# Kernel tuning notes

Hardware: AMD Instinct MI355X
Metric: run time of the kernel (lower is better)

## Reference

```python
import jax, jax.numpy as jnp
import numpy as np

N_CANONICAL = 16
D_IN, D_HID, D_OUT = 784, 128, 10
BATCH = 65536


def setup_inputs() -> dict:
    key = jax.random.key(0)
    ks = jax.random.split(key, 6)
    x = jax.random.normal(ks[0], (BATCH, D_IN), dtype=jnp.float32)
    # per-canonical Linear params (PyTorch Linear: y = x @ W.T + b)
    s1 = 1.0 / np.sqrt(D_IN)
    s2 = 1.0 / np.sqrt(D_HID)
    fc_w = jax.random.uniform(ks[1], (N_CANONICAL, D_HID, D_IN), jnp.float32, -s1, s1)
    fc_b = jax.random.uniform(ks[2], (N_CANONICAL, D_HID), jnp.float32, -s1, s1)
    cls_w = jax.random.uniform(ks[3], (N_CANONICAL, D_OUT, D_HID), jnp.float32, -s2, s2)
    cls_b = jax.random.uniform(ks[4], (N_CANONICAL, D_OUT), jnp.float32, -s2, s2)
    factor = jnp.full((N_CANONICAL,), 1.0 / N_CANONICAL, dtype=jnp.float32)
    return {"x": x, "fc_w": fc_w, "fc_b": fc_b, "cls_w": cls_w, "cls_b": cls_b, "factor": factor}


def reference(x, fc_w, fc_b, cls_w, cls_b, factor):
    # x: [B, 784] (already flattened view of 28x28)
    # Ensemble of Linears combined by learned scalar factor. Since the combination
    # is linear, pre-combine weights: sum_k factor[k] * W_k (same math, fused GEMM).
    w1 = jnp.einsum('k,kod->od', factor, fc_w)   # [128, 784]
    b1 = factor @ fc_b                           # [128]
    h = jax.nn.relu(x @ w1.T + b1)               # [B, 128]
    w2 = jnp.einsum('k,kod->od', factor, cls_w)  # [10, 128]
    b2 = factor @ cls_b                          # [10]
    out = h @ w2.T + b2                          # [B, 10]
    return out
```

## Files before the change

### kernel.cpp

```cpp
#include <hip/hip_runtime.h>
#include <hip/hip_bf16.h>

typedef __attribute__((ext_vector_type(8))) short short8;
typedef __attribute__((ext_vector_type(4))) float f32x4;

#define N_ENS 16
#define D_IN 784
#define D_HID 128
#define D_OUT 10
#define KPAD 800
#define NKT 25
#define BM 64
#define TILE_B_BYTES 8192
#define WS_B1 204800
#define WS_W2 205312
#define WS_B2 210432

__device__ __forceinline__ unsigned short f2bf(float f) {
  unsigned int u = __float_as_uint(f);
  return (unsigned short)((u + 0x7FFFu + ((u >> 16) & 1u)) >> 16);
}

__device__ __forceinline__ void gload_lds16(const void* g, void* l) {
  __builtin_amdgcn_global_load_lds((const __attribute__((address_space(1))) void*)g,
                                   (__attribute__((address_space(3))) void*)l, 16, 0, 0);
}

__device__ __forceinline__ int swz(int row, int byte_in_row) {
  return ((row << 6) | byte_in_row) ^ ((row & 7) << 4);
}

__global__ void prep_kernel(const float* __restrict__ fc_w, const float* __restrict__ fc_b,
                            const float* __restrict__ cls_w, const float* __restrict__ cls_b,
                            const float* __restrict__ factor, char* __restrict__ ws) {
  int tid = blockIdx.x * 256 + threadIdx.x;
  float f[N_ENS];
#pragma unroll
  for (int e = 0; e < N_ENS; ++e) f[e] = factor[e];

  if (tid < D_HID * KPAD) {
    int col = tid / KPAD;
    int k   = tid - col * KPAD;
    float v = 0.f;
    if (k < D_IN) {
#pragma unroll
      for (int e = 0; e < N_ENS; ++e) v += f[e] * fc_w[(size_t)(e * D_HID + col) * D_IN + k];
    }
    int kt = k >> 5, kk = k & 31;
    *(unsigned short*)(ws + kt * TILE_B_BYTES + swz(col, kk * 2)) = f2bf(v);
  } else if (tid < D_HID * KPAD + D_HID) {
    int col = tid - D_HID * KPAD;
    float v = 0.f;
#pragma unroll
    for (int e = 0; e < N_ENS; ++e) v += f[e] * fc_b[e * D_HID + col];
    *(float*)(ws + WS_B1 + col * 4) = v;
  } else if (tid < D_HID * KPAD + D_HID + D_HID * D_OUT) {
    int i = tid - (D_HID * KPAD + D_HID);
    int n = i / D_OUT, o = i - n * D_OUT;
    float v = 0.f;
#pragma unroll
    for (int e = 0; e < N_ENS; ++e) v += f[e] * cls_w[(e * D_OUT + o) * D_HID + n];
    *(float*)(ws + WS_W2 + i * 4) = v;
  } else if (tid < D_HID * KPAD + D_HID + D_HID * D_OUT + D_OUT) {
    int o = tid - (D_HID * KPAD + D_HID + D_HID * D_OUT);
    float v = 0.f;
#pragma unroll
    for (int e = 0; e < N_ENS; ++e) v += f[e] * cls_b[e * D_OUT + o];
    *(float*)(ws + WS_B2 + o * 4) = v;
  }
}

__global__ __launch_bounds__(256, 4) void mnist_fused(const float* __restrict__ x,
                                                      const char* __restrict__ ws,
                                                      float* __restrict__ out) {
  __shared__ char smem[35584];
  const int tid = threadIdx.x;
  const int lane = tid & 63;
  const int w  = tid >> 6;
  const int wr = w >> 1, wc = w & 1;
  const int kg = lane >> 4, l15 = lane & 15;
  const int m0 = blockIdx.x * BM;

  const int arow = tid >> 2, aq = tid & 3;
  const float* xrow = x + (size_t)(m0 + arow) * D_IN;
  const int awbyte = swz(arow, aq << 4);

  f32x4 acc[2][4];
#pragma unroll
  for (int mi = 0; mi < 2; ++mi)
#pragma unroll
    for (int ni = 0; ni < 4; ++ni) acc[mi][ni] = f32x4{0.f, 0.f, 0.f, 0.f};

  float xv[8];

  {
    const float4 v0 = *(const float4*)(xrow + aq * 8);
    const float4 v1 = *(const float4*)(xrow + aq * 8 + 4);
    xv[0]=v0.x; xv[1]=v0.y; xv[2]=v0.z; xv[3]=v0.w;
    xv[4]=v1.x; xv[5]=v1.y; xv[6]=v1.z; xv[7]=v1.w;
  }
#pragma unroll
  for (int i = 0; i < 2; ++i)
    gload_lds16(ws + w * 2048 + i * 1024 + lane * 16, smem + 8192 + w * 2048 + i * 1024);
  {
    union { unsigned short u[8]; short8 s; } pk;
#pragma unroll
    for (int j = 0; j < 8; ++j) pk.u[j] = f2bf(xv[j]);
    *(short8*)(smem + awbyte) = pk.s;
  }
  __syncthreads();

  for (int kt = 0; kt < NKT; ++kt) {
    const int cur = kt & 1, nb = cur ^ 1;
    const bool more = (kt + 1) < NKT;
    if (more) {
      const int ktn = kt + 1;
#pragma unroll
      for (int i = 0; i < 2; ++i)
        gload_lds16(ws + ktn * TILE_B_BYTES + w * 2048 + i * 1024 + lane * 16,
                    smem + 8192 + nb * 8192 + w * 2048 + i * 1024);
      const int k0 = ktn * 32 + aq * 8;
      if (k0 < D_IN) {
        const float4 v0 = *(const float4*)(xrow + k0);
        const float4 v1 = *(const float4*)(xrow + k0 + 4);
        xv[0]=v0.x; xv[1]=v0.y; xv[2]=v0.z; xv[3]=v0.w;
        xv[4]=v1.x; xv[5]=v1.y; xv[6]=v1.z; xv[7]=v1.w;
      } else {
#pragma unroll
        for (int j = 0; j < 8; ++j) xv[j] = 0.f;
      }
    }
    {
      const char* Ab = smem + cur * 4096;
      const char* Bb = smem + 8192 + cur * 8192;
      short8 a[2], b[4];
#pragma unroll
      for (int mi = 0; mi < 2; ++mi) {
        const int r = wr * 32 + mi * 16 + l15;
        a[mi] = *(const short8*)(Ab + swz(r, kg << 4));
      }
#pragma unroll
      for (int ni = 0; ni < 4; ++ni) {
        const int c = wc * 64 + ni * 16 + l15;
        b[ni] = *(const short8*)(Bb + swz(c, kg << 4));
      }
#pragma unroll
      for (int mi = 0; mi < 2; ++mi)
#pragma unroll
        for (int ni = 0; ni < 4; ++ni)
          acc[mi][ni] = __builtin_amdgcn_mfma_f32_16x16x32_bf16(a[mi], b[ni], acc[mi][ni], 0, 0, 0);
    }
    if (more) {
      union { unsigned short u[8]; short8 s; } pk;
#pragma unroll
      for (int j = 0; j < 8; ++j) pk.u[j] = f2bf(xv[j]);
      *(short8*)(smem + nb * 4096 + awbyte) = pk.s;
    }
    __syncthreads();
  }

  const float* b1 = (const float*)(ws + WS_B1);
  float* h = (float*)smem;
#pragma unroll
  for (int ni = 0; ni < 4; ++ni) {
    const int n = wc * 64 + ni * 16 + l15;
    const float bv = b1[n];
#pragma unroll
    for (int mi = 0; mi < 2; ++mi) {
      const int rb = wr * 32 + mi * 16 + kg * 4;
#pragma unroll
      for (int j = 0; j < 4; ++j) {
        float v = acc[mi][ni][j] + bv;
        h[(rb + j) * 129 + n] = v > 0.f ? v : 0.f;
      }
    }
  }
  __syncthreads();

  const float* w2t = (const float*)(ws + WS_W2);
  const float* b2  = (const float*)(ws + WS_B2);
  float po[10];
#pragma unroll
  for (int o = 0; o < 10; ++o) po[o] = 0.f;
  const int m = tid & 63;
  const int half = (tid >> 6) & 1;
  if (tid < 128) {
    const float* hr  = h + m * 129 + half * 64;
    const float* wr2 = w2t + half * 64 * D_OUT;
    for (int n = 0; n < 64; ++n) {
      const float hv = hr[n];
#pragma unroll
      for (int o = 0; o < 10; ++o) po[o] += hv * wr2[n * 10 + o];
    }
  }
  float* red = (float*)(smem + 33024);
  if (tid >= 64 && tid < 128) {
#pragma unroll
    for (int o = 0; o < 10; ++o) red[m * 10 + o] = po[o];
  }
  __syncthreads();
  if (tid < 64) {
    float* op = out + (size_t)(m0 + m) * 10;
#pragma unroll
    for (int o = 0; o < 10; o += 2) {
      float2 v;
      v.x = po[o]     + red[m * 10 + o]     + b2[o];
      v.y = po[o + 1] + red[m * 10 + o + 1] + b2[o + 1];
      *(float2*)(op + o) = v;
    }
  }
}

extern "C" void kernel_launch(void* const* d_in, const int* in_sizes, int n_in,
                              void* d_out, int out_size, void* d_ws, size_t ws_size,
                              hipStream_t stream) {
  const float* x      = (const float*)d_in[0];
  const float* fc_w   = (const float*)d_in[1];
  const float* fc_b   = (const float*)d_in[2];
  const float* cls_w  = (const float*)d_in[3];
  const float* cls_b  = (const float*)d_in[4];
  const float* factor = (const float*)d_in[5];
  char* ws = (char*)d_ws;
  float* outp = (float*)d_out;

  prep_kernel<<<406, 256, 0, stream>>>(fc_w, fc_b, cls_w, cls_b, factor, ws);
  mnist_fused<<<1024, 256, 0, stream>>>(x, ws, outp);
}
```

Before: 49.09 us.

## Load GEMM operands directly from global into registers, drop LDS staging and block syncs

Each wave now owns 16 rows and all 128 hidden columns. It reads x straight from global into registers and converts it to bf16 for the MFMA A operand. It also reads the prepacked bf16 weights directly from global (L2) instead of double-buffering them through LDS, which removes the per-k-step __syncthreads. The second layer is computed per wave from a small LDS copy of the transposed classifier weights, with shuffle reductions, so all threads take part and the partial-sum exchange through LDS goes away. The trade-off is that every wave refetches the full weight tile from cache and has less latency hiding without explicit prefetch.

```diff
diff --git a/kernel.cpp b/kernel.cpp
--- a/kernel.cpp
+++ b/kernel.cpp
@@ -10,8 +10,7 @@
 #define D_OUT 10
 #define KPAD 800
 #define NKT 25
-#define BM 64
-#define TILE_B_BYTES 8192
+#define TILE_B 8192
 #define WS_B1 204800
 #define WS_W2 205312
 #define WS_B2 210432
@@ -19,15 +18,6 @@
 __device__ __forceinline__ unsigned short f2bf(float f) {
   unsigned int u = __float_as_uint(f);
   return (unsigned short)((u + 0x7FFFu + ((u >> 16) & 1u)) >> 16);
-}
-
-__device__ __forceinline__ void gload_lds16(const void* g, void* l) {
-  __builtin_amdgcn_global_load_lds((const __attribute__((address_space(1))) void*)g,
-                                   (__attribute__((address_space(3))) void*)l, 16, 0, 0);
-}
-
-__device__ __forceinline__ int swz(int row, int byte_in_row) {
-  return ((row << 6) | byte_in_row) ^ ((row & 7) << 4);
 }
 
 __global__ void prep_kernel(const float* __restrict__ fc_w, const float* __restrict__ fc_b,
@@ -47,7 +37,8 @@
       for (int e = 0; e < N_ENS; ++e) v += f[e] * fc_w[(size_t)(e * D_HID + col) * D_IN + k];
     }
     int kt = k >> 5, kk = k & 31;
-    *(unsigned short*)(ws + kt * TILE_B_BYTES + swz(col, kk * 2)) = f2bf(v);
+    int byte = kt * TILE_B + col * 64 + ((kk >> 3) << 4) + ((kk & 7) << 1);
+    *(unsigned short*)(ws + byte) = f2bf(v);
   } else if (tid < D_HID * KPAD + D_HID) {
     int col = tid - D_HID * KPAD;
     float v = 0.f;
@@ -56,7 +47,7 @@
     *(float*)(ws + WS_B1 + col * 4) = v;
   } else if (tid < D_HID * KPAD + D_HID + D_HID * D_OUT) {
     int i = tid - (D_HID * KPAD + D_HID);
-    int n = i / D_OUT, o = i - n * D_OUT;
+    int o = i >> 7, n = i & 127;
     float v = 0.f;
 #pragma unroll
     for (int e = 0; e < N_ENS; ++e) v += f[e] * cls_w[(e * D_OUT + o) * D_HID + n];
@@ -73,139 +64,98 @@
 __global__ __launch_bounds__(256, 4) void mnist_fused(const float* __restrict__ x,
                                                       const char* __restrict__ ws,
                                                       float* __restrict__ out) {
-  __shared__ char smem[35584];
-  const int tid = threadIdx.x;
+  __shared__ float h[64][132];
+  __shared__ float w2s[10][128];
+  const int tid  = threadIdx.x;
   const int lane = tid & 63;
-  const int w  = tid >> 6;
-  const int wr = w >> 1, wc = w & 1;
-  const int kg = lane >> 4, l15 = lane & 15;
-  const int m0 = blockIdx.x * BM;
-
-  const int arow = tid >> 2, aq = tid & 3;
-  const float* xrow = x + (size_t)(m0 + arow) * D_IN;
-  const int awbyte = swz(arow, aq << 4);
-
-  f32x4 acc[2][4];
-#pragma unroll
-  for (int mi = 0; mi < 2; ++mi)
-#pragma unroll
-    for (int ni = 0; ni < 4; ++ni) acc[mi][ni] = f32x4{0.f, 0.f, 0.f, 0.f};
-
-  float xv[8];
+  const int w    = tid >> 6;
+  const int l15  = lane & 15;
+  const int kg   = lane >> 4;
+  const int m0   = blockIdx.x * 64;
 
   {
-    const float4 v0 = *(const float4*)(xrow + aq * 8);
-    const float4 v1 = *(const float4*)(xrow + aq * 8 + 4);
-    xv[0]=v0.x; xv[1]=v0.y; xv[2]=v0.z; xv[3]=v0.w;
-    xv[4]=v1.x; xv[5]=v1.y; xv[6]=v1.z; xv[7]=v1.w;
-  }
-#pragma unroll
-  for (int i = 0; i < 2; ++i)
-    gload_lds16(ws + w * 2048 + i * 1024 + lane * 16, smem + 8192 + w * 2048 + i * 1024);
-  {
-    union { unsigned short u[8]; short8 s; } pk;
-#pragma unroll
-    for (int j = 0; j < 8; ++j) pk.u[j] = f2bf(xv[j]);
-    *(short8*)(smem + awbyte) = pk.s;
+    const float* w2g = (const float*)(ws + WS_W2);
+    for (int i = tid; i < 1280; i += 256) ((float*)w2s)[i] = w2g[i];
   }
   __syncthreads();
 
-  for (int kt = 0; kt < NKT; ++kt) {
-    const int cur = kt & 1, nb = cur ^ 1;
-    const bool more = (kt + 1) < NKT;
-    if (more) {
-      const int ktn = kt + 1;
+  const float* ar = x + (size_t)(m0 + w * 16 + l15) * D_IN;
+  const char*  bb = ws + l15 * 64 + kg * 16;
+
+  f32x4 acc[8];
 #pragma unroll
-      for (int i = 0; i < 2; ++i)
-        gload_lds16(ws + ktn * TILE_B_BYTES + w * 2048 + i * 1024 + lane * 16,
-                    smem + 8192 + nb * 8192 + w * 2048 + i * 1024);
-      const int k0 = ktn * 32 + aq * 8;
-      if (k0 < D_IN) {
-        const float4 v0 = *(const float4*)(xrow + k0);
-        const float4 v1 = *(const float4*)(xrow + k0 + 4);
-        xv[0]=v0.x; xv[1]=v0.y; xv[2]=v0.z; xv[3]=v0.w;
-        xv[4]=v1.x; xv[5]=v1.y; xv[6]=v1.z; xv[7]=v1.w;
-      } else {
+  for (int ni = 0; ni < 8; ++ni) acc[ni] = f32x4{0.f, 0.f, 0.f, 0.f};
+
+#pragma unroll 2
+  for (int kt = 0; kt < 24; ++kt) {
+    const float4 a0 = *(const float4*)(ar + kt * 32 + kg * 8);
+    const float4 a1 = *(const float4*)(ar + kt * 32 + kg * 8 + 4);
+    short8 b[8];
 #pragma unroll
-        for (int j = 0; j < 8; ++j) xv[j] = 0.f;
-      }
+    for (int ni = 0; ni < 8; ++ni)
+      b[ni] = *(const short8*)(bb + kt * TILE_B + ni * 1024);
+    union { unsigned short u[8]; short8 s; } pk;
+    pk.u[0] = f2bf(a0.x); pk.u[1] = f2bf(a0.y); pk.u[2] = f2bf(a0.z); pk.u[3] = f2bf(a0.w);
+    pk.u[4] = f2bf(a1.x); pk.u[5] = f2bf(a1.y); pk.u[6] = f2bf(a1.z); pk.u[7] = f2bf(a1.w);
+#pragma unroll
+    for (int ni = 0; ni < 8; ++ni)
+      acc[ni] = __builtin_amdgcn_mfma_f32_16x16x32_bf16(pk.s, b[ni], acc[ni], 0, 0, 0);
+  }
+  {
+    float4 a0 = float4{0.f, 0.f, 0.f, 0.f}, a1 = float4{0.f, 0.f, 0.f, 0.f};
+    if (kg < 2) {
+      a0 = *(const float4*)(ar + 768 + kg * 8);
+      a1 = *(const float4*)(ar + 768 + kg * 8 + 4);
     }
-    {
-      const char* Ab = smem + cur * 4096;
-      const char* Bb = smem + 8192 + cur * 8192;
-      short8 a[2], b[4];
+    short8 b[8];
 #pragma unroll
-      for (int mi = 0; mi < 2; ++mi) {
-        const int r = wr * 32 + mi * 16 + l15;
-        a[mi] = *(const short8*)(Ab + swz(r, kg << 4));
-      }
+    for (int ni = 0; ni < 8; ++ni)
+      b[ni] = *(const short8*)(bb + 24 * TILE_B + ni * 1024);
+    union { unsigned short u[8]; short8 s; } pk;
+    pk.u[0] = f2bf(a0.x); pk.u[1] = f2bf(a0.y); pk.u[2] = f2bf(a0.z); pk.u[3] = f2bf(a0.w);
+    pk.u[4] = f2bf(a1.x); pk.u[5] = f2bf(a1.y); pk.u[6] = f2bf(a1.z); pk.u[7] = f2bf(a1.w);
 #pragma unroll
-      for (int ni = 0; ni < 4; ++ni) {
-        const int c = wc * 64 + ni * 16 + l15;
-        b[ni] = *(const short8*)(Bb + swz(c, kg << 4));
-      }
-#pragma unroll
-      for (int mi = 0; mi < 2; ++mi)
-#pragma unroll
-        for (int ni = 0; ni < 4; ++ni)
-          acc[mi][ni] = __builtin_amdgcn_mfma_f32_16x16x32_bf16(a[mi], b[ni], acc[mi][ni], 0, 0, 0);
-    }
-    if (more) {
-      union { unsigned short u[8]; short8 s; } pk;
-#pragma unroll
-      for (int j = 0; j < 8; ++j) pk.u[j] = f2bf(xv[j]);
-      *(short8*)(smem + nb * 4096 + awbyte) = pk.s;
-    }
-    __syncthreads();
+    for (int ni = 0; ni < 8; ++ni)
+      acc[ni] = __builtin_amdgcn_mfma_f32_16x16x32_bf16(pk.s, b[ni], acc[ni], 0, 0, 0);
   }
 
-  const float* b1 = (const float*)(ws + WS_B1);
-  float* h = (float*)smem;
+  const float* b1g = (const float*)(ws + WS_B1);
 #pragma unroll
-  for (int ni = 0; ni < 4; ++ni) {
-    const int n = wc * 64 + ni * 16 + l15;
-    const float bv = b1[n];
+  for (int ni = 0; ni < 8; ++ni) {
+    const float bv = b1g[ni * 16 + l15];
 #pragma unroll
-    for (int mi = 0; mi < 2; ++mi) {
-      const int rb = wr * 32 + mi * 16 + kg * 4;
-#pragma unroll
-      for (int j = 0; j < 4; ++j) {
-        float v = acc[mi][ni][j] + bv;
-        h[(rb + j) * 129 + n] = v > 0.f ? v : 0.f;
-      }
+    for (int j = 0; j < 4; ++j) {
+      float v = acc[ni][j] + bv;
+      h[w * 16 + kg * 4 + j][ni * 16 + l15] = v > 0.f ? v : 0.f;
     }
   }
-  __syncthreads();
 
-  const float* w2t = (const float*)(ws + WS_W2);
-  const float* b2  = (const float*)(ws + WS_B2);
+  const int row = w * 16 + l15;
   float po[10];
 #pragma unroll
   for (int o = 0; o < 10; ++o) po[o] = 0.f;
-  const int m = tid & 63;
-  const int half = (tid >> 6) & 1;
-  if (tid < 128) {
-    const float* hr  = h + m * 129 + half * 64;
-    const float* wr2 = w2t + half * 64 * D_OUT;
-    for (int n = 0; n < 64; ++n) {
-      const float hv = hr[n];
 #pragma unroll
-      for (int o = 0; o < 10; ++o) po[o] += hv * wr2[n * 10 + o];
+  for (int n4 = 0; n4 < 8; ++n4) {
+    const float4 hv = *(const float4*)(&h[row][kg * 32 + n4 * 4]);
+#pragma unroll
+    for (int o = 0; o < 10; ++o) {
+      const float4 wv = *(const float4*)(&w2s[o][kg * 32 + n4 * 4]);
+      po[o] += hv.x * wv.x + hv.y * wv.y + hv.z * wv.z + hv.w * wv.w;
     }
   }
-  float* red = (float*)(smem + 33024);
-  if (tid >= 64 && tid < 128) {
 #pragma unroll
-    for (int o = 0; o < 10; ++o) red[m * 10 + o] = po[o];
+  for (int o = 0; o < 10; ++o) {
+    po[o] += __shfl_xor(po[o], 16);
+    po[o] += __shfl_xor(po[o], 32);
   }
-  __syncthreads();
-  if (tid < 64) {
-    float* op = out + (size_t)(m0 + m) * 10;
+  if (kg == 0) {
+    const float* b2g = (const float*)(ws + WS_B2);
+    float* op = out + (size_t)(m0 + row) * 10;
 #pragma unroll
     for (int o = 0; o < 10; o += 2) {
       float2 v;
-      v.x = po[o]     + red[m * 10 + o]     + b2[o];
-      v.y = po[o + 1] + red[m * 10 + o + 1] + b2[o + 1];
+      v.x = po[o]     + b2g[o];
+      v.y = po[o + 1] + b2g[o + 1];
       *(float2*)(op + o) = v;
     }
   }
```

Result: slower. 74.35 us (+51.5%).
